# Optimization experiments

Hardware: AMD Instinct MI355X
Metric: run time of the kernel (lower is better)

## Reference

```python
import jax, jax.numpy as jnp
import numpy as np

B, N, C, H = 2, 2048, 512, 8
D = C // H  # head dim = 64
SCALE = C ** -0.5  # module uses heads_channels**-0.5 (full inner dim, not per-head)


def setup_inputs() -> dict:
    key = jax.random.key(0)
    ks = jax.random.split(key, 9)
    return {
        "q": jax.random.normal(ks[0], (B, N, C), jnp.float32),
        "kv": jax.random.normal(ks[1], (B, N, C), jnp.float32),
        "pos_q": jax.random.normal(ks[2], (B, N, D), jnp.float32),
        "pos_k": jax.random.normal(ks[3], (B, N, D), jnp.float32),
        "Wq": jax.random.normal(ks[4], (C, C), jnp.float32) * (C ** -0.5),
        "Wk": jax.random.normal(ks[5], (C, C), jnp.float32) * (C ** -0.5),
        "Wv": jax.random.normal(ks[6], (C, C), jnp.float32) * (C ** -0.5),
        "Wo": jax.random.normal(ks[7], (C, C), jnp.float32) * (C ** -0.5),
        "bo": jnp.zeros((C,), jnp.float32),
    }


def reference(q, kv, pos_q, pos_k, Wq, Wk, Wv, Wo, bo):
    # projections: [b n c] @ [c c] -> [b n c]
    qp = q @ Wq
    kp = kv @ Wk
    vp = kv @ Wv
    # split heads: b n (h d) -> b h n d
    split = lambda t: t.reshape(B, N, H, D).transpose(0, 2, 1, 3)
    qh, kh, vh = split(qp), split(kp), split(vp)
    # additive positional bias, broadcast over heads: b n d -> b 1 n d
    qh = qh + pos_q[:, None, :, :]
    kh = kh + pos_k[:, None, :, :]
    sim = jnp.einsum("bhid,bhjd->bhij", qh, kh) * SCALE
    attn = jax.nn.softmax(sim, axis=-1)
    out = jnp.einsum("bhij,bhjd->bhid", attn, vh)
    # merge heads: b h n d -> b n (h d)
    out = out.transpose(0, 2, 1, 3).reshape(B, N, C)
    return out @ Wo + bo
```

## Files before the change

kernel.cpp:

```cpp
#include <hip/hip_runtime.h>
#include <hip/hip_bf16.h>
#include <stdint.h>
#include <math.h>

static constexpr int kB = 2, kN = 2048, kC = 512, kH = 8, kD = 64;
static constexpr float kScaleL2E =
    (float)(0.044194173824159216 * 1.4426950408889634);
static constexpr float kShift = 12.0f;

typedef short bf16x8 __attribute__((ext_vector_type(8)));
typedef short bf16x4 __attribute__((ext_vector_type(4)));
typedef float f32x4  __attribute__((ext_vector_type(4)));

__device__ __forceinline__ float bf2f(unsigned short u) {
  union { unsigned int i; float f; } v; v.i = ((unsigned int)u) << 16; return v.f;
}
__device__ __forceinline__ unsigned short f2bf(float f) {
  union { float f; unsigned int i; } v; v.f = f;
  unsigned int x = v.i;
  return (unsigned short)((x + 0x7FFFu + ((x >> 16) & 1u)) >> 16);
}
__device__ __forceinline__ short f2bs(float f) { return (short)f2bf(f); }
__device__ __forceinline__ unsigned int pack2_t(float lo, float hi) {
  union { float f; unsigned int i; } a, b; a.f = lo; b.f = hi;
  return (b.i & 0xFFFF0000u) | (a.i >> 16);
}

__global__ __launch_bounds__(256) void prep_kernel(
    const float* __restrict__ q, const float* __restrict__ kv,
    const float* __restrict__ Wq, const float* __restrict__ Wk,
    const float* __restrict__ Wv,
    unsigned short* __restrict__ qbf, unsigned short* __restrict__ kvbf,
    unsigned short* __restrict__ wT)
{
  const int t = threadIdx.x;
  if (blockIdx.z == 0) {
    const int gid = blockIdx.x * 256 + t;
    #pragma unroll
    for (int it = 0; it < 8; ++it) {
      int i4 = gid + it * 65536;
      float4 a = *(const float4*)(q + (size_t)i4 * 4);
      float4 b = *(const float4*)(kv + (size_t)i4 * 4);
      bf16x4 ab = {f2bs(a.x), f2bs(a.y), f2bs(a.z), f2bs(a.w)};
      bf16x4 bb = {f2bs(b.x), f2bs(b.y), f2bs(b.z), f2bs(b.w)};
      *(bf16x4*)(qbf + (size_t)i4 * 4) = ab;
      *(bf16x4*)(kvbf + (size_t)i4 * 4) = bb;
    }
  } else {
    if (blockIdx.x >= 192) return;
    const int wsel = blockIdx.x >> 6;
    const int tile = blockIdx.x & 63;
    const int tr = tile >> 3, tc = tile & 7;
    const float* W = (wsel == 0) ? Wq : (wsel == 1 ? Wk : Wv);
    unsigned short* out = wT + (size_t)wsel * kC * kC;

    __shared__ __align__(16) float Ts[64][68];
    #pragma unroll
    for (int it = 0; it < 4; ++it) {
      int e = t + it * 256;
      int r = e >> 4, c4 = (e & 15) * 4;
      *(float4*)&Ts[r][c4] =
          *(const float4*)(W + (size_t)(tr * 64 + r) * kC + tc * 64 + c4);
    }
    __syncthreads();
    const int n = t >> 2, ks = (t & 3) * 16;
    unsigned short* orow = out + (size_t)(tc * 64 + n) * kC + tr * 64 + ks;
    #pragma unroll
    for (int c = 0; c < 4; ++c) {
      ushort4 o;
      o.x = f2bf(Ts[ks + c * 4 + 0][n]);
      o.y = f2bf(Ts[ks + c * 4 + 1][n]);
      o.z = f2bf(Ts[ks + c * 4 + 2][n]);
      o.w = f2bf(Ts[ks + c * 4 + 3][n]);
      *(ushort4*)(orow + c * 4) = o;
    }
  }
}

__global__ __launch_bounds__(256) void proj_kernel(
    const unsigned short* __restrict__ qbf,
    const unsigned short* __restrict__ kvbf,
    const unsigned short* __restrict__ wT,
    const float* __restrict__ pos_q,
    const float* __restrict__ pos_k,
    unsigned short* __restrict__ qh,
    unsigned short* __restrict__ kh,
    unsigned short* __restrict__ vhT)
{
  const int z = blockIdx.z;
  const unsigned short* A = (z == 0) ? qbf : kvbf;
  const unsigned short* Bt = wT + (size_t)z * kC * kC;

  __shared__ __align__(16) unsigned short As[128][72];
  __shared__ __align__(16) unsigned short Bs[64][72];

  const int t = threadIdx.x;
  const int w = t >> 6, lane = t & 63;
  const int l15 = lane & 15, quad = lane >> 4;
  const int m0 = blockIdx.x * 128;
  const int n0 = blockIdx.y * 64;

  const int sr = t >> 3, sc = (t & 7) * 8;

  bf16x8 pa[4], pb[2];
  #pragma unroll
  for (int i = 0; i < 4; ++i)
    pa[i] = *(const bf16x8*)(A + (size_t)(m0 + sr + i * 32) * kC + sc);
  #pragma unroll
  for (int i = 0; i < 2; ++i)
    pb[i] = *(const bf16x8*)(Bt + (size_t)(n0 + sr + i * 32) * kC + sc);

  f32x4 acc[2][4];
  #pragma unroll
  for (int si = 0; si < 2; ++si)
    #pragma unroll
    for (int ct = 0; ct < 4; ++ct) acc[si][ct] = (f32x4){0.f, 0.f, 0.f, 0.f};

  for (int k0 = 0; k0 < kC; k0 += 64) {
    if (k0) __syncthreads();
    #pragma unroll
    for (int i = 0; i < 4; ++i) *(bf16x8*)&As[sr + i * 32][sc] = pa[i];
    #pragma unroll
    for (int i = 0; i < 2; ++i) *(bf16x8*)&Bs[sr + i * 32][sc] = pb[i];
    __syncthreads();
    if (k0 + 64 < kC) {
      int kn = k0 + 64;
      #pragma unroll
      for (int i = 0; i < 4; ++i)
        pa[i] = *(const bf16x8*)(A + (size_t)(m0 + sr + i * 32) * kC + kn + sc);
      #pragma unroll
      for (int i = 0; i < 2; ++i)
        pb[i] = *(const bf16x8*)(Bt + (size_t)(n0 + sr + i * 32) * kC + kn + sc);
    }
    bf16x8 a0[2], a1[2];
    #pragma unroll
    for (int si = 0; si < 2; ++si) {
      a0[si] = *(const bf16x8*)&As[w * 32 + si * 16 + l15][quad * 8];
      a1[si] = *(const bf16x8*)&As[w * 32 + si * 16 + l15][32 + quad * 8];
    }
    #pragma unroll
    for (int ct = 0; ct < 4; ++ct) {
      bf16x8 b0 = *(const bf16x8*)&Bs[ct * 16 + l15][quad * 8];
      bf16x8 b1 = *(const bf16x8*)&Bs[ct * 16 + l15][32 + quad * 8];
      #pragma unroll
      for (int si = 0; si < 2; ++si) {
        acc[si][ct] = __builtin_amdgcn_mfma_f32_16x16x32_bf16(a0[si], b0, acc[si][ct], 0, 0, 0);
        acc[si][ct] = __builtin_amdgcn_mfma_f32_16x16x32_bf16(a1[si], b1, acc[si][ct], 0, 0, 0);
      }
    }
  }

  const int h = n0 >> 6;
  #pragma unroll
  for (int si = 0; si < 2; ++si)
    #pragma unroll
    for (int r = 0; r < 4; ++r) {
      int m = m0 + w * 32 + si * 16 + quad * 4 + r;
      int b = m >> 11, n_seq = m & (kN - 1);
      #pragma unroll
      for (int ct = 0; ct < 4; ++ct) {
        int d = ct * 16 + l15;
        float val = acc[si][ct][r];
        if (z == 2) {
          vhT[(((size_t)b * kH + h) * kD + d) * kN + n_seq] = f2bf(val);
        } else if (z == 0) {
          val = (val + pos_q[((size_t)b * kN + n_seq) * kD + d]) * kScaleL2E;
          qh[(((size_t)b * kH + h) * kN + n_seq) * kD + d] = f2bf(val);
        } else {
          val = val + pos_k[((size_t)b * kN + n_seq) * kD + d];
          kh[(((size_t)b * kH + h) * kN + n_seq) * kD + d] = f2bf(val);
        }
      }
    }
}

__global__ __launch_bounds__(256, 4) void attn_kernel(
    const unsigned short* __restrict__ qh,
    const unsigned short* __restrict__ kh,
    const unsigned short* __restrict__ vhT,
    unsigned short* __restrict__ o0,
    unsigned short* __restrict__ o1,
    float* __restrict__ lbuf)
{
  const int bh = blockIdx.y;
  const int b = bh >> 3, h = bh & 7;
  const int q0 = blockIdx.x * 64;
  const int s = blockIdx.z;
  const int kbase = s * 1024;
  const int t = threadIdx.x;
  const int w = t >> 6, lane = t & 63;
  const int l15 = lane & 15, quad = lane >> 4;

  __shared__ __align__(16) unsigned short Kbf[2][64][72];
  __shared__ __align__(16) unsigned short Vt[2][64][72];

  const unsigned short* Qb = qh  + (size_t)bh * kN * kD;
  const unsigned short* Kb = kh  + (size_t)bh * kN * kD;
  const unsigned short* Vb = vhT + (size_t)bh * kD * kN;

  const unsigned short* qrow = Qb + (size_t)(q0 + w * 16 + l15) * kD;
  bf16x8 aq0 = *(const bf16x8*)(qrow + quad * 8);
  bf16x8 aq1 = *(const bf16x8*)(qrow + 32 + quad * 8);

  const int sr = t >> 3, sc = (t & 7) * 8, sr2 = sr + 32;

  bf16x8 pk0 = *(const bf16x8*)(Kb + (size_t)(kbase + sr) * kD + sc);
  bf16x8 pk1 = *(const bf16x8*)(Kb + (size_t)(kbase + sr2) * kD + sc);
  bf16x8 pv0 = *(const bf16x8*)(Vb + (size_t)sr * kN + kbase + sc);
  bf16x8 pv1 = *(const bf16x8*)(Vb + (size_t)sr2 * kN + kbase + sc);
  *(bf16x8*)&Kbf[0][sr][sc]  = pk0;
  *(bf16x8*)&Kbf[0][sr2][sc] = pk1;
  *(bf16x8*)&Vt[0][sr][sc]   = pv0;
  *(bf16x8*)&Vt[0][sr2][sc]  = pv1;
  {
    int kt1 = kbase + 64;
    pk0 = *(const bf16x8*)(Kb + (size_t)(kt1 + sr) * kD + sc);
    pk1 = *(const bf16x8*)(Kb + (size_t)(kt1 + sr2) * kD + sc);
    pv0 = *(const bf16x8*)(Vb + (size_t)sr * kN + kt1 + sc);
    pv1 = *(const bf16x8*)(Vb + (size_t)sr2 * kN + kt1 + sc);
  }

  f32x4 o[4];
  #pragma unroll
  for (int nt = 0; nt < 4; ++nt) o[nt] = (f32x4){0.f, 0.f, 0.f, 0.f};
  float l_run = 0.f;

  const int src_a = l15 + 32 * (quad & 1);
  const int src_b = src_a + 16;
  const bool hi_sel = (quad & 2) != 0;

  for (int i = 0; i < 16; ++i) {
    __syncthreads();
    if (i + 1 < 16) {
      unsigned short (*Kw)[72] = Kbf[(i + 1) & 1];
      unsigned short (*Vw)[72] = Vt[(i + 1) & 1];
      *(bf16x8*)&Kw[sr][sc]  = pk0;
      *(bf16x8*)&Kw[sr2][sc] = pk1;
      *(bf16x8*)&Vw[sr][sc]  = pv0;
      *(bf16x8*)&Vw[sr2][sc] = pv1;
      if (i + 2 < 16) {
        int ktn = kbase + (i + 2) * 64;
        pk0 = *(const bf16x8*)(Kb + (size_t)(ktn + sr) * kD + sc);
        pk1 = *(const bf16x8*)(Kb + (size_t)(ktn + sr2) * kD + sc);
        pv0 = *(const bf16x8*)(Vb + (size_t)sr * kN + ktn + sc);
        pv1 = *(const bf16x8*)(Vb + (size_t)sr2 * kN + ktn + sc);
      }
    }
    const unsigned short (*Kr)[72] = Kbf[i & 1];
    const unsigned short (*Vr)[72] = Vt[i & 1];

    f32x4 sacc[4];
    #pragma unroll
    for (int ct = 0; ct < 4; ++ct) {
      bf16x8 ak0 = *(const bf16x8*)&Kr[ct * 16 + l15][quad * 8];
      bf16x8 ak1 = *(const bf16x8*)&Kr[ct * 16 + l15][32 + quad * 8];
      f32x4 zz = (f32x4){0.f, 0.f, 0.f, 0.f};
      zz = __builtin_amdgcn_mfma_f32_16x16x32_bf16(ak0, aq0, zz, 0, 0, 0);
      zz = __builtin_amdgcn_mfma_f32_16x16x32_bf16(ak1, aq1, zz, 0, 0, 0);
      sacc[ct] = zz;
    }

    float psum = 0.f;
    #pragma unroll
    for (int ct = 0; ct < 4; ++ct)
      #pragma unroll
      for (int r = 0; r < 4; ++r) {
        float p = exp2f(sacc[ct][r] - kShift);
        sacc[ct][r] = p;
        psum += p;
      }
    psum += __shfl_xor(psum, 16);
    psum += __shfl_xor(psum, 32);
    l_run += psum;

    unsigned int pk01[4], pk23[4];
    #pragma unroll
    for (int ct = 0; ct < 4; ++ct) {
      pk01[ct] = pack2_t(sacc[ct][0], sacc[ct][1]);
      pk23[ct] = pack2_t(sacc[ct][2], sacc[ct][3]);
    }
    unsigned int s01a[4], s23a[4], s01b[4], s23b[4];
    #pragma unroll
    for (int ct = 0; ct < 4; ++ct) {
      s01a[ct] = (unsigned int)__shfl((int)pk01[ct], src_a);
      s23a[ct] = (unsigned int)__shfl((int)pk23[ct], src_a);
      s01b[ct] = (unsigned int)__shfl((int)pk01[ct], src_b);
      s23b[ct] = (unsigned int)__shfl((int)pk23[ct], src_b);
    }
    union { unsigned int u[4]; bf16x8 v; } pf0, pf1;
    pf0.u[0] = hi_sel ? s01a[1] : s01a[0];
    pf0.u[1] = hi_sel ? s23a[1] : s23a[0];
    pf0.u[2] = hi_sel ? s01b[1] : s01b[0];
    pf0.u[3] = hi_sel ? s23b[1] : s23b[0];
    pf1.u[0] = hi_sel ? s01a[3] : s01a[2];
    pf1.u[1] = hi_sel ? s23a[3] : s23a[2];
    pf1.u[2] = hi_sel ? s01b[3] : s01b[2];
    pf1.u[3] = hi_sel ? s23b[3] : s23b[2];

    #pragma unroll
    for (int nt = 0; nt < 4; ++nt) {
      bf16x8 av0 = *(const bf16x8*)&Vr[nt * 16 + l15][quad * 8];
      bf16x8 av1 = *(const bf16x8*)&Vr[nt * 16 + l15][32 + quad * 8];
      o[nt] = __builtin_amdgcn_mfma_f32_16x16x32_bf16(av0, pf0.v, o[nt], 0, 0, 0);
      o[nt] = __builtin_amdgcn_mfma_f32_16x16x32_bf16(av1, pf1.v, o[nt], 0, 0, 0);
    }
  }

  unsigned short* od = s ? o1 : o0;
  const int n = q0 + w * 16 + l15;
  unsigned short* obase = od + ((size_t)b * kN + n) * kC + h * kD + quad * 4;
  #pragma unroll
  for (int nt = 0; nt < 4; ++nt) {
    ushort4 st;
    st.x = f2bf(o[nt][0]);
    st.y = f2bf(o[nt][1]);
    st.z = f2bf(o[nt][2]);
    st.w = f2bf(o[nt][3]);
    *(ushort4*)(obase + nt * 16) = st;
  }
  if (quad == 0) lbuf[(size_t)(s * 16 + bh) * kN + n] = l_run;
}

__global__ __launch_bounds__(256) void combine_kernel(
    unsigned short* __restrict__ o0,
    const unsigned short* __restrict__ o1,
    const float* __restrict__ lbuf)
{
  const size_t f = ((size_t)blockIdx.x * 256 + threadIdx.x) * 8;
  const int c = (int)(f & (kC - 1));
  const int n = (int)((f >> 9) & (kN - 1));
  const int b = (int)(f >> 20);
  const int bh = b * 8 + (c >> 6);
  float l0 = lbuf[(size_t)bh * kN + n];
  float l1 = lbuf[(size_t)(16 + bh) * kN + n];
  float wgt = 1.f / (l0 + l1);
  bf16x8 x = *(bf16x8*)(o0 + f);
  bf16x8 y = *(const bf16x8*)(o1 + f);
  bf16x8 r;
  #pragma unroll
  for (int j = 0; j < 8; ++j) {
    float v = (bf2f((unsigned short)x[j]) + bf2f((unsigned short)y[j])) * wgt;
    r[j] = (short)f2bf(v);
  }
  *(bf16x8*)(o0 + f) = r;
}

__global__ __launch_bounds__(256) void proj_out_kernel(
    const unsigned short* __restrict__ ao,
    const float* __restrict__ Wo,
    const float* __restrict__ bo,
    float* __restrict__ out)
{
  __shared__ __align__(16) unsigned short Wt[64][72];

  const int t = threadIdx.x;
  const int w = t >> 6, lane = t & 63;
  const int l15 = lane & 15, quad = lane >> 4;
  const int m0 = blockIdx.x * 64;
  const int n0 = blockIdx.y * 64;

  const unsigned short* arow = ao + (size_t)(m0 + w * 16 + l15) * kC;

  ushort4 pw[4];
  #pragma unroll
  for (int i = 0; i < 4; ++i) {
    int e = t + i * 256;
    int r = e >> 4, c4 = (e & 15) * 4;
    float4 wv = *(const float4*)(Wo + (size_t)r * kC + n0 + c4);
    pw[i] = make_ushort4(f2bf(wv.x), f2bf(wv.y), f2bf(wv.z), f2bf(wv.w));
  }
  bf16x8 pa0 = *(const bf16x8*)(arow + quad * 8);
  bf16x8 pa1 = *(const bf16x8*)(arow + 32 + quad * 8);

  f32x4 acc[4];
  #pragma unroll
  for (int ct = 0; ct < 4; ++ct) acc[ct] = (f32x4){0.f, 0.f, 0.f, 0.f};

  for (int k0 = 0; k0 < kC; k0 += 64) {
    if (k0) __syncthreads();
    #pragma unroll
    for (int i = 0; i < 4; ++i) {
      int e = t + i * 256;
      int r = e >> 4, c4 = (e & 15) * 4;
      Wt[c4 + 0][r] = pw[i].x;
      Wt[c4 + 1][r] = pw[i].y;
      Wt[c4 + 2][r] = pw[i].z;
      Wt[c4 + 3][r] = pw[i].w;
    }
    __syncthreads();
    bf16x8 a0 = pa0, a1 = pa1;
    if (k0 + 64 < kC) {
      int kn = k0 + 64;
      #pragma unroll
      for (int i = 0; i < 4; ++i) {
        int e = t + i * 256;
        int r = e >> 4, c4 = (e & 15) * 4;
        float4 wv = *(const float4*)(Wo + (size_t)(kn + r) * kC + n0 + c4);
        pw[i] = make_ushort4(f2bf(wv.x), f2bf(wv.y), f2bf(wv.z), f2bf(wv.w));
      }
      pa0 = *(const bf16x8*)(arow + kn + quad * 8);
      pa1 = *(const bf16x8*)(arow + kn + 32 + quad * 8);
    }
    #pragma unroll
    for (int ct = 0; ct < 4; ++ct) {
      bf16x8 b0 = *(const bf16x8*)&Wt[ct * 16 + l15][quad * 8];
      bf16x8 b1 = *(const bf16x8*)&Wt[ct * 16 + l15][32 + quad * 8];
      acc[ct] = __builtin_amdgcn_mfma_f32_16x16x32_bf16(a0, b0, acc[ct], 0, 0, 0);
      acc[ct] = __builtin_amdgcn_mfma_f32_16x16x32_bf16(a1, b1, acc[ct], 0, 0, 0);
    }
  }

  #pragma unroll
  for (int ct = 0; ct < 4; ++ct) {
    int n = n0 + ct * 16 + l15;
    float bb = bo[n];
    #pragma unroll
    for (int r = 0; r < 4; ++r) {
      int m = m0 + w * 16 + quad * 4 + r;
      out[(size_t)m * kC + n] = acc[ct][r] + bb;
    }
  }
}

extern "C" void kernel_launch(void* const* d_in, const int* in_sizes, int n_in,
                              void* d_out, int out_size, void* d_ws, size_t ws_size,
                              hipStream_t stream) {
  (void)in_sizes; (void)n_in; (void)out_size; (void)ws_size;
  const float* q     = (const float*)d_in[0];
  const float* kv    = (const float*)d_in[1];
  const float* pos_q = (const float*)d_in[2];
  const float* pos_k = (const float*)d_in[3];
  const float* Wq    = (const float*)d_in[4];
  const float* Wk    = (const float*)d_in[5];
  const float* Wv    = (const float*)d_in[6];
  const float* Wo    = (const float*)d_in[7];
  const float* bo    = (const float*)d_in[8];
  float* out = (float*)d_out;

  const size_t seg = (size_t)kB * kH * kN * kD;

  unsigned short* qbf = (unsigned short*)d_ws;
  unsigned short* qhp = qbf + seg;
  unsigned short* khp = qhp + seg;
  unsigned short* vtp = khp + seg;
  unsigned short* o0p = qbf;
  unsigned short* aop = qbf;

  unsigned short* kvbf = (unsigned short*)d_out;
  unsigned short* wT   = kvbf + seg;
  unsigned short* o1p  = kvbf;
  float*          lbp  = (float*)(kvbf + seg);

  dim3 blk(256);
  prep_kernel<<<dim3(256, 1, 2), blk, 0, stream>>>(q, kv, Wq, Wk, Wv, qbf, kvbf, wT);
  proj_kernel<<<dim3(32, 8, 3), blk, 0, stream>>>(qbf, kvbf, wT, pos_q, pos_k,
                                                  qhp, khp, vtp);
  attn_kernel<<<dim3(32, 16, 2), blk, 0, stream>>>(qhp, khp, vtp, o0p, o1p, lbp);
  combine_kernel<<<dim3(1024), blk, 0, stream>>>(o0p, o1p, lbp);
  proj_out_kernel<<<dim3(64, 8), blk, 0, stream>>>(aop, Wo, bo, out);
}
```

Measured before the change: 166.9 us.

## Fuse K/V projections sharing A tile and double query rows per attention block

The projection kernel now computes K and V together in one block, so the kv activation tile is loaded once and reused for two weight tiles, and the grid drops from three z-slices to two. The attention kernel processes 128 query rows per block (two 16-row groups per wave), so each K/V tile loaded to shared memory serves twice as many queries. The cost is higher register pressure, a lower launch_bounds occupancy hint, and half as many attention blocks, which may leave CUs underfilled. The q-projection blocks now sit idle beside heavier kv blocks, making the load imbalanced.

```diff
diff --git a/kernel.cpp b/kernel.cpp
--- a/kernel.cpp
+++ b/kernel.cpp
@@ -87,12 +87,13 @@
     unsigned short* __restrict__ kh,
     unsigned short* __restrict__ vhT)
 {
-  const int z = blockIdx.z;
-  const unsigned short* A = (z == 0) ? qbf : kvbf;
-  const unsigned short* Bt = wT + (size_t)z * kC * kC;
+  const bool kvmode = (blockIdx.z == 1);
+  const unsigned short* A = kvmode ? kvbf : qbf;
+  const unsigned short* Bt0 = wT + (kvmode ? (size_t)kC * kC : 0);
+  const unsigned short* Bt1 = wT + 2 * (size_t)kC * kC;
 
   __shared__ __align__(16) unsigned short As[128][72];
-  __shared__ __align__(16) unsigned short Bs[64][72];
+  __shared__ __align__(16) unsigned short Bs[2][64][72];
 
   const int t = threadIdx.x;
   const int w = t >> 6, lane = t & 63;
@@ -102,26 +103,36 @@
 
   const int sr = t >> 3, sc = (t & 7) * 8;
 
-  bf16x8 pa[4], pb[2];
+  bf16x8 pa[4], pb0[2], pb1[2];
   #pragma unroll
   for (int i = 0; i < 4; ++i)
     pa[i] = *(const bf16x8*)(A + (size_t)(m0 + sr + i * 32) * kC + sc);
   #pragma unroll
   for (int i = 0; i < 2; ++i)
-    pb[i] = *(const bf16x8*)(Bt + (size_t)(n0 + sr + i * 32) * kC + sc);
-
-  f32x4 acc[2][4];
+    pb0[i] = *(const bf16x8*)(Bt0 + (size_t)(n0 + sr + i * 32) * kC + sc);
+  if (kvmode)
+    #pragma unroll
+    for (int i = 0; i < 2; ++i)
+      pb1[i] = *(const bf16x8*)(Bt1 + (size_t)(n0 + sr + i * 32) * kC + sc);
+
+  f32x4 acc0[2][4], acc1[2][4];
   #pragma unroll
   for (int si = 0; si < 2; ++si)
     #pragma unroll
-    for (int ct = 0; ct < 4; ++ct) acc[si][ct] = (f32x4){0.f, 0.f, 0.f, 0.f};
+    for (int ct = 0; ct < 4; ++ct) {
+      acc0[si][ct] = (f32x4){0.f, 0.f, 0.f, 0.f};
+      acc1[si][ct] = (f32x4){0.f, 0.f, 0.f, 0.f};
+    }
 
   for (int k0 = 0; k0 < kC; k0 += 64) {
     if (k0) __syncthreads();
     #pragma unroll
     for (int i = 0; i < 4; ++i) *(bf16x8*)&As[sr + i * 32][sc] = pa[i];
     #pragma unroll
-    for (int i = 0; i < 2; ++i) *(bf16x8*)&Bs[sr + i * 32][sc] = pb[i];
+    for (int i = 0; i < 2; ++i) *(bf16x8*)&Bs[0][sr + i * 32][sc] = pb0[i];
+    if (kvmode)
+      #pragma unroll
+      for (int i = 0; i < 2; ++i) *(bf16x8*)&Bs[1][sr + i * 32][sc] = pb1[i];
     __syncthreads();
     if (k0 + 64 < kC) {
       int kn = k0 + 64;
@@ -130,7 +141,11 @@
         pa[i] = *(const bf16x8*)(A + (size_t)(m0 + sr + i * 32) * kC + kn + sc);
       #pragma unroll
       for (int i = 0; i < 2; ++i)
-        pb[i] = *(const bf16x8*)(Bt + (size_t)(n0 + sr + i * 32) * kC + kn + sc);
+        pb0[i] = *(const bf16x8*)(Bt0 + (size_t)(n0 + sr + i * 32) * kC + kn + sc);
+      if (kvmode)
+        #pragma unroll
+        for (int i = 0; i < 2; ++i)
+          pb1[i] = *(const bf16x8*)(Bt1 + (size_t)(n0 + sr + i * 32) * kC + kn + sc);
     }
     bf16x8 a0[2], a1[2];
     #pragma unroll
@@ -140,12 +155,21 @@
     }
     #pragma unroll
     for (int ct = 0; ct < 4; ++ct) {
-      bf16x8 b0 = *(const bf16x8*)&Bs[ct * 16 + l15][quad * 8];
-      bf16x8 b1 = *(const bf16x8*)&Bs[ct * 16 + l15][32 + quad * 8];
+      bf16x8 b0 = *(const bf16x8*)&Bs[0][ct * 16 + l15][quad * 8];
+      bf16x8 b1 = *(const bf16x8*)&Bs[0][ct * 16 + l15][32 + quad * 8];
       #pragma unroll
       for (int si = 0; si < 2; ++si) {
-        acc[si][ct] = __builtin_amdgcn_mfma_f32_16x16x32_bf16(a0[si], b0, acc[si][ct], 0, 0, 0);
-        acc[si][ct] = __builtin_amdgcn_mfma_f32_16x16x32_bf16(a1[si], b1, acc[si][ct], 0, 0, 0);
+        acc0[si][ct] = __builtin_amdgcn_mfma_f32_16x16x32_bf16(a0[si], b0, acc0[si][ct], 0, 0, 0);
+        acc0[si][ct] = __builtin_amdgcn_mfma_f32_16x16x32_bf16(a1[si], b1, acc0[si][ct], 0, 0, 0);
+      }
+      if (kvmode) {
+        bf16x8 c0 = *(const bf16x8*)&Bs[1][ct * 16 + l15][quad * 8];
+        bf16x8 c1 = *(const bf16x8*)&Bs[1][ct * 16 + l15][32 + quad * 8];
+        #pragma unroll
+        for (int si = 0; si < 2; ++si) {
+          acc1[si][ct] = __builtin_amdgcn_mfma_f32_16x16x32_bf16(a0[si], c0, acc1[si][ct], 0, 0, 0);
+          acc1[si][ct] = __builtin_amdgcn_mfma_f32_16x16x32_bf16(a1[si], c1, acc1[si][ct], 0, 0, 0);
+        }
       }
     }
   }
@@ -160,21 +184,20 @@
       #pragma unroll
       for (int ct = 0; ct < 4; ++ct) {
         int d = ct * 16 + l15;
-        float val = acc[si][ct][r];
-        if (z == 2) {
-          vhT[(((size_t)b * kH + h) * kD + d) * kN + n_seq] = f2bf(val);
-        } else if (z == 0) {
-          val = (val + pos_q[((size_t)b * kN + n_seq) * kD + d]) * kScaleL2E;
+        if (!kvmode) {
+          float val = (acc0[si][ct][r] +
+                       pos_q[((size_t)b * kN + n_seq) * kD + d]) * kScaleL2E;
           qh[(((size_t)b * kH + h) * kN + n_seq) * kD + d] = f2bf(val);
         } else {
-          val = val + pos_k[((size_t)b * kN + n_seq) * kD + d];
-          kh[(((size_t)b * kH + h) * kN + n_seq) * kD + d] = f2bf(val);
+          float vk = acc0[si][ct][r] + pos_k[((size_t)b * kN + n_seq) * kD + d];
+          kh[(((size_t)b * kH + h) * kN + n_seq) * kD + d] = f2bf(vk);
+          vhT[(((size_t)b * kH + h) * kD + d) * kN + n_seq] = f2bf(acc1[si][ct][r]);
         }
       }
     }
 }
 
-__global__ __launch_bounds__(256, 4) void attn_kernel(
+__global__ __launch_bounds__(256, 2) void attn_kernel(
     const unsigned short* __restrict__ qh,
     const unsigned short* __restrict__ kh,
     const unsigned short* __restrict__ vhT,
@@ -184,7 +207,7 @@
 {
   const int bh = blockIdx.y;
   const int b = bh >> 3, h = bh & 7;
-  const int q0 = blockIdx.x * 64;
+  const int q0 = blockIdx.x * 128;
   const int s = blockIdx.z;
   const int kbase = s * 1024;
   const int t = threadIdx.x;
@@ -198,9 +221,13 @@
   const unsigned short* Kb = kh  + (size_t)bh * kN * kD;
   const unsigned short* Vb = vhT + (size_t)bh * kD * kN;
 
-  const unsigned short* qrow = Qb + (size_t)(q0 + w * 16 + l15) * kD;
-  bf16x8 aq0 = *(const bf16x8*)(qrow + quad * 8);
-  bf16x8 aq1 = *(const bf16x8*)(qrow + 32 + quad * 8);
+  bf16x8 aq[2][2];
+  #pragma unroll
+  for (int g = 0; g < 2; ++g) {
+    const unsigned short* qrow = Qb + (size_t)(q0 + w * 32 + g * 16 + l15) * kD;
+    aq[g][0] = *(const bf16x8*)(qrow + quad * 8);
+    aq[g][1] = *(const bf16x8*)(qrow + 32 + quad * 8);
+  }
 
   const int sr = t >> 3, sc = (t & 7) * 8, sr2 = sr + 32;
 
@@ -220,10 +247,12 @@
     pv1 = *(const bf16x8*)(Vb + (size_t)sr2 * kN + kt1 + sc);
   }
 
-  f32x4 o[4];
-  #pragma unroll
-  for (int nt = 0; nt < 4; ++nt) o[nt] = (f32x4){0.f, 0.f, 0.f, 0.f};
-  float l_run = 0.f;
+  f32x4 o[2][4];
+  #pragma unroll
+  for (int g = 0; g < 2; ++g)
+    #pragma unroll
+    for (int nt = 0; nt < 4; ++nt) o[g][nt] = (f32x4){0.f, 0.f, 0.f, 0.f};
+  float l_run[2] = {0.f, 0.f};
 
   const int src_a = l15 + 32 * (quad & 1);
   const int src_b = src_a + 16;
@@ -249,76 +278,88 @@
     const unsigned short (*Kr)[72] = Kbf[i & 1];
     const unsigned short (*Vr)[72] = Vt[i & 1];
 
-    f32x4 sacc[4];
+    f32x4 sacc[2][4];
     #pragma unroll
     for (int ct = 0; ct < 4; ++ct) {
       bf16x8 ak0 = *(const bf16x8*)&Kr[ct * 16 + l15][quad * 8];
       bf16x8 ak1 = *(const bf16x8*)&Kr[ct * 16 + l15][32 + quad * 8];
-      f32x4 zz = (f32x4){0.f, 0.f, 0.f, 0.f};
-      zz = __builtin_amdgcn_mfma_f32_16x16x32_bf16(ak0, aq0, zz, 0, 0, 0);
-      zz = __builtin_amdgcn_mfma_f32_16x16x32_bf16(ak1, aq1, zz, 0, 0, 0);
-      sacc[ct] = zz;
-    }
-
-    float psum = 0.f;
-    #pragma unroll
-    for (int ct = 0; ct < 4; ++ct)
-      #pragma unroll
-      for (int r = 0; r < 4; ++r) {
-        float p = exp2f(sacc[ct][r] - kShift);
-        sacc[ct][r] = p;
-        psum += p;
-      }
-    psum += __shfl_xor(psum, 16);
-    psum += __shfl_xor(psum, 32);
-    l_run += psum;
-
-    unsigned int pk01[4], pk23[4];
-    #pragma unroll
-    for (int ct = 0; ct < 4; ++ct) {
-      pk01[ct] = pack2_t(sacc[ct][0], sacc[ct][1]);
-      pk23[ct] = pack2_t(sacc[ct][2], sacc[ct][3]);
-    }
-    unsigned int s01a[4], s23a[4], s01b[4], s23b[4];
-    #pragma unroll
-    for (int ct = 0; ct < 4; ++ct) {
-      s01a[ct] = (unsigned int)__shfl((int)pk01[ct], src_a);
-      s23a[ct] = (unsigned int)__shfl((int)pk23[ct], src_a);
-      s01b[ct] = (unsigned int)__shfl((int)pk01[ct], src_b);
-      s23b[ct] = (unsigned int)__shfl((int)pk23[ct], src_b);
-    }
-    union { unsigned int u[4]; bf16x8 v; } pf0, pf1;
-    pf0.u[0] = hi_sel ? s01a[1] : s01a[0];
-    pf0.u[1] = hi_sel ? s23a[1] : s23a[0];
-    pf0.u[2] = hi_sel ? s01b[1] : s01b[0];
-    pf0.u[3] = hi_sel ? s23b[1] : s23b[0];
-    pf1.u[0] = hi_sel ? s01a[3] : s01a[2];
-    pf1.u[1] = hi_sel ? s23a[3] : s23a[2];
-    pf1.u[2] = hi_sel ? s01b[3] : s01b[2];
-    pf1.u[3] = hi_sel ? s23b[3] : s23b[2];
+      #pragma unroll
+      for (int g = 0; g < 2; ++g) {
+        f32x4 zz = (f32x4){0.f, 0.f, 0.f, 0.f};
+        zz = __builtin_amdgcn_mfma_f32_16x16x32_bf16(ak0, aq[g][0], zz, 0, 0, 0);
+        zz = __builtin_amdgcn_mfma_f32_16x16x32_bf16(ak1, aq[g][1], zz, 0, 0, 0);
+        sacc[g][ct] = zz;
+      }
+    }
+
+    union PF { unsigned int u[4]; bf16x8 v; } pf[2][2];
+    #pragma unroll
+    for (int g = 0; g < 2; ++g) {
+      float psum = 0.f;
+      #pragma unroll
+      for (int ct = 0; ct < 4; ++ct)
+        #pragma unroll
+        for (int r = 0; r < 4; ++r) {
+          float p = exp2f(sacc[g][ct][r] - kShift);
+          sacc[g][ct][r] = p;
+          psum += p;
+        }
+      psum += __shfl_xor(psum, 16);
+      psum += __shfl_xor(psum, 32);
+      l_run[g] += psum;
+
+      unsigned int pk01[4], pk23[4];
+      #pragma unroll
+      for (int ct = 0; ct < 4; ++ct) {
+        pk01[ct] = pack2_t(sacc[g][ct][0], sacc[g][ct][1]);
+        pk23[ct] = pack2_t(sacc[g][ct][2], sacc[g][ct][3]);
+      }
+      unsigned int s01a[4], s23a[4], s01b[4], s23b[4];
+      #pragma unroll
+      for (int ct = 0; ct < 4; ++ct) {
+        s01a[ct] = (unsigned int)__shfl((int)pk01[ct], src_a);
+        s23a[ct] = (unsigned int)__shfl((int)pk23[ct], src_a);
+        s01b[ct] = (unsigned int)__shfl((int)pk01[ct], src_b);
+        s23b[ct] = (unsigned int)__shfl((int)pk23[ct], src_b);
+      }
+      pf[g][0].u[0] = hi_sel ? s01a[1] : s01a[0];
+      pf[g][0].u[1] = hi_sel ? s23a[1] : s23a[0];
+      pf[g][0].u[2] = hi_sel ? s01b[1] : s01b[0];
+      pf[g][0].u[3] = hi_sel ? s23b[1] : s23b[0];
+      pf[g][1].u[0] = hi_sel ? s01a[3] : s01a[2];
+      pf[g][1].u[1] = hi_sel ? s23a[3] : s23a[2];
+      pf[g][1].u[2] = hi_sel ? s01b[3] : s01b[2];
+      pf[g][1].u[3] = hi_sel ? s23b[3] : s23b[2];
+    }
 
     #pragma unroll
     for (int nt = 0; nt < 4; ++nt) {
       bf16x8 av0 = *(const bf16x8*)&Vr[nt * 16 + l15][quad * 8];
       bf16x8 av1 = *(const bf16x8*)&Vr[nt * 16 + l15][32 + quad * 8];
-      o[nt] = __builtin_amdgcn_mfma_f32_16x16x32_bf16(av0, pf0.v, o[nt], 0, 0, 0);
-      o[nt] = __builtin_amdgcn_mfma_f32_16x16x32_bf16(av1, pf1.v, o[nt], 0, 0, 0);
+      #pragma unroll
+      for (int g = 0; g < 2; ++g) {
+        o[g][nt] = __builtin_amdgcn_mfma_f32_16x16x32_bf16(av0, pf[g][0].v, o[g][nt], 0, 0, 0);
+        o[g][nt] = __builtin_amdgcn_mfma_f32_16x16x32_bf16(av1, pf[g][1].v, o[g][nt], 0, 0, 0);
+      }
     }
   }
 
   unsigned short* od = s ? o1 : o0;
-  const int n = q0 + w * 16 + l15;
-  unsigned short* obase = od + ((size_t)b * kN + n) * kC + h * kD + quad * 4;
-  #pragma unroll
-  for (int nt = 0; nt < 4; ++nt) {
-    ushort4 st;
-    st.x = f2bf(o[nt][0]);
-    st.y = f2bf(o[nt][1]);
-    st.z = f2bf(o[nt][2]);
-    st.w = f2bf(o[nt][3]);
-    *(ushort4*)(obase + nt * 16) = st;
-  }
-  if (quad == 0) lbuf[(size_t)(s * 16 + bh) * kN + n] = l_run;
+  #pragma unroll
+  for (int g = 0; g < 2; ++g) {
+    const int n = q0 + w * 32 + g * 16 + l15;
+    unsigned short* obase = od + ((size_t)b * kN + n) * kC + h * kD + quad * 4;
+    #pragma unroll
+    for (int nt = 0; nt < 4; ++nt) {
+      ushort4 st;
+      st.x = f2bf(o[g][nt][0]);
+      st.y = f2bf(o[g][nt][1]);
+      st.z = f2bf(o[g][nt][2]);
+      st.w = f2bf(o[g][nt][3]);
+      *(ushort4*)(obase + nt * 16) = st;
+    }
+    if (quad == 0) lbuf[(size_t)(s * 16 + bh) * kN + n] = l_run[g];
+  }
 }
 
 __global__ __launch_bounds__(256) void combine_kernel(
@@ -453,9 +494,9 @@
 
   dim3 blk(256);
   prep_kernel<<<dim3(256, 1, 2), blk, 0, stream>>>(q, kv, Wq, Wk, Wv, qbf, kvbf, wT);
-  proj_kernel<<<dim3(32, 8, 3), blk, 0, stream>>>(qbf, kvbf, wT, pos_q, pos_k,
+  proj_kernel<<<dim3(32, 8, 2), blk, 0, stream>>>(qbf, kvbf, wT, pos_q, pos_k,
                                                   qhp, khp, vtp);
-  attn_kernel<<<dim3(32, 16, 2), blk, 0, stream>>>(qhp, khp, vtp, o0p, o1p, lbp);
+  attn_kernel<<<dim3(16, 16, 2), blk, 0, stream>>>(qhp, khp, vtp, o0p, o1p, lbp);
   combine_kernel<<<dim3(1024), blk, 0, stream>>>(o0p, o1p, lbp);
   proj_out_kernel<<<dim3(64, 8), blk, 0, stream>>>(aop, Wo, bo, out);
 }
```

After: 167.2 us. Within noise of the previous version (+0.2%).
